# Optimization experiments

Hardware: AMD Instinct MI355X
Metric: run time of the kernel (lower is better)

Reference implementation:

```python
import jax, jax.numpy as jnp
import numpy as np

DIM = 1024
NUM_HEADS = 16
NUM_KV_HEADS = 2
HEAD_DIM = DIM // NUM_HEADS          # 64
REPEATS = NUM_HEADS // NUM_KV_HEADS  # 8
WINDOW = 256
HALF = WINDOW // 2                   # 128
BATCH, SEQ = 2, 2048


def setup_inputs() -> dict:
    key = jax.random.key(0)
    ks = jax.random.split(key, 9)
    sc = 1.0 / np.sqrt(DIM)
    return {
        "x":  jax.random.normal(ks[0], (BATCH, SEQ, DIM), jnp.float32),
        "Wq": jax.random.normal(ks[1], (DIM, NUM_HEADS * HEAD_DIM), jnp.float32) * sc,
        "bq": jax.random.normal(ks[2], (NUM_HEADS * HEAD_DIM,), jnp.float32) * 0.01,
        "Wk": jax.random.normal(ks[3], (DIM, NUM_KV_HEADS * HEAD_DIM), jnp.float32) * sc,
        "bk": jax.random.normal(ks[4], (NUM_KV_HEADS * HEAD_DIM,), jnp.float32) * 0.01,
        "Wv": jax.random.normal(ks[5], (DIM, NUM_KV_HEADS * HEAD_DIM), jnp.float32) * sc,
        "bv": jax.random.normal(ks[6], (NUM_KV_HEADS * HEAD_DIM,), jnp.float32) * 0.01,
        "Wo": jax.random.normal(ks[7], (DIM, DIM), jnp.float32) * sc,
        "bo": jax.random.normal(ks[8], (DIM,), jnp.float32) * 0.01,
    }


def reference(x, Wq, bq, Wk, bk, Wv, bv, Wo, bo):
    # Training-path GQA sliding-window attention (faithful to the torch module):
    #  - K/V zero-padded by HALF on each side of the sequence; window of size
    #    WINDOW centered on each query position (unfold with step 1).
    #  - NOTE (faithful): the original code builds mask = tril(ones)[-1], which is
    #    an all-ones row, so masked_fill is a no-op -> NO causal mask inside the
    #    window; padded positions contribute score 0 (not -inf) to the softmax.
    #  - NOTE (faithful): the training path does NOT scale scores by 1/sqrt(d).
    b, s, _ = x.shape
    q = (x @ Wq + bq).reshape(b, s, NUM_HEADS, HEAD_DIM).transpose(0, 2, 1, 3)      # [b,H,s,d]
    k = (x @ Wk + bk).reshape(b, s, NUM_KV_HEADS, HEAD_DIM).transpose(0, 2, 1, 3)   # [b,G,s,d]
    v = (x @ Wv + bv).reshape(b, s, NUM_KV_HEADS, HEAD_DIM).transpose(0, 2, 1, 3)

    kp = jnp.pad(k, ((0, 0), (0, 0), (HALF, HALF), (0, 0)))  # [b,G,s+W,d]
    vp = jnp.pad(v, ((0, 0), (0, 0), (HALF, HALF), (0, 0)))

    # window gather indices: window i covers padded positions [i, i+W)
    idx = jnp.arange(s)[:, None] + jnp.arange(WINDOW)[None, :]  # [s,W]
    k_win = kp[:, :, idx]  # [b,G,s,W,d]  (gather at kv-head granularity, not H)
    v_win = vp[:, :, idx]

    # group query heads by kv head: head h -> kv group h // REPEATS
    qg = q.reshape(b, NUM_KV_HEADS, REPEATS, s, HEAD_DIM)        # [b,G,r,s,d]
    scores = jnp.einsum('bgrsd,bgswd->bgrsw', qg, k_win)         # no scaling (faithful)
    probs = jax.nn.softmax(scores, axis=-1)
    out = jnp.einsum('bgrsw,bgswd->bgrsd', probs, v_win)         # [b,G,r,s,d]

    out = out.reshape(b, NUM_HEADS, s, HEAD_DIM).transpose(0, 2, 1, 3).reshape(b, s, DIM)
    return out @ Wo + bo
```

## Files before the change

### kernel.cpp

```cpp
#include <hip/hip_runtime.h>
#include <hip/hip_fp16.h>

typedef _Float16 h16;
typedef __attribute__((ext_vector_type(8))) _Float16 h16x8;
typedef __attribute__((ext_vector_type(4))) float f32x4;

#define DIM   1024
#define SEQ   2048
#define NKV   2
#define HD    64
#define HALFW 128
#define NQKV  1280
#define KSTG  288
#define KCOLS 272
#define VCOLS 304
#define VSTR  312

__global__ void preprocess_kernel(const float* __restrict__ x,
                                  const float* __restrict__ bq,
                                  const float* __restrict__ bk,
                                  const float* __restrict__ bv,
                                  const float* __restrict__ Wq,
                                  const float* __restrict__ Wk,
                                  const float* __restrict__ Wv,
                                  const float* __restrict__ Wo,
                                  h16* __restrict__ xh, float* __restrict__ bqkv,
                                  h16* __restrict__ wqkvt, h16* __restrict__ wot)
{
    __shared__ float tile[32][33];
    const int tid = threadIdx.x;
    const int blk = blockIdx.x;
    if (blk < 2048) {
        int i = blk * 256 + tid;
        size_t base = (size_t)i * 8;
        float4 a = *(const float4*)(x + base);
        float4 b = *(const float4*)(x + base + 4);
        h16x8 o = { (h16)a.x,(h16)a.y,(h16)a.z,(h16)a.w,
                    (h16)b.x,(h16)b.y,(h16)b.z,(h16)b.w };
        *(h16x8*)(xh + base) = o;
        if (i < NQKV) {
            float v = (i < DIM) ? bq[i] : (i < DIM+128 ? bk[i-DIM] : bv[i-DIM-128]);
            bqkv[i] = v;
        }
        return;
    }
    const int tx = tid & 31, ty = tid >> 5;
    if (blk < 2048 + 1280) {
        int bid = blk - 2048;
        int n0 = (bid % 40) * 32, k0 = (bid / 40) * 32;
        const float* src; int ldn, noff;
        if (n0 < DIM)          { src = Wq; ldn = DIM; noff = n0; }
        else if (n0 < DIM+128) { src = Wk; ldn = 128; noff = n0 - DIM; }
        else                   { src = Wv; ldn = 128; noff = n0 - DIM - 128; }
#pragma unroll
        for (int i = 0; i < 4; ++i)
            tile[ty + 8*i][tx] = src[(size_t)(k0 + ty + 8*i)*ldn + noff + tx];
        __syncthreads();
#pragma unroll
        for (int i = 0; i < 4; ++i)
            wqkvt[(size_t)(n0 + ty + 8*i)*DIM + k0 + tx] = (h16)tile[tx][ty + 8*i];
    } else {
        int bid = blk - 3328;
        int n0 = (bid % 32) * 32, k0 = (bid / 32) * 32;
#pragma unroll
        for (int i = 0; i < 4; ++i)
            tile[ty + 8*i][tx] = Wo[(size_t)(k0 + ty + 8*i)*DIM + n0 + tx];
        __syncthreads();
#pragma unroll
        for (int i = 0; i < 4; ++i)
            wot[(size_t)(n0 + ty + 8*i)*DIM + k0 + tx] = (h16)tile[tx][ty + 8*i];
    }
}

template<int MODE>
__global__ __launch_bounds__(256, 2)
void gemm_kernel(const h16* __restrict__ A, const h16* __restrict__ Bt,
                 const float* __restrict__ bias,
                 h16* __restrict__ qo, h16* __restrict__ ko, h16* __restrict__ vto,
                 float* __restrict__ co, int K, int nx)
{
    __shared__ __align__(16) h16 As[2][128*64];
    __shared__ __align__(16) h16 Bs[2][128*64];
    const int nwg = gridDim.x, bid = blockIdx.x;
    const int q8 = nwg >> 3, r8 = nwg & 7, xcd = bid & 7, off = bid >> 3;
    const int wg = (xcd < r8 ? xcd*(q8+1) : r8*(q8+1) + (xcd-r8)*q8) + off;
    const int m0 = (wg / nx) * 128, n0 = (wg % nx) * 128;
    const int tid = threadIdx.x, lane = tid & 63, wid = tid >> 6;
    const int wr = wid >> 1, wc = wid & 1;
    f32x4 acc[4][4] = {};

    auto stage = [&](int buf, int kk) {
#pragma unroll
        for (int i = 0; i < 4; ++i) {
            int slot = i*256 + tid;
            int row = slot >> 3;
            int scol = ((slot & 7) ^ (row & 7)) * 8;
            __builtin_amdgcn_global_load_lds(
                (const __attribute__((address_space(1))) void*)(A + (size_t)(m0 + row)*K + kk + scol),
                (__attribute__((address_space(3))) void*)(&As[buf][slot*8]), 16, 0, 0);
            __builtin_amdgcn_global_load_lds(
                (const __attribute__((address_space(1))) void*)(Bt + (size_t)(n0 + row)*K + kk + scol),
                (__attribute__((address_space(3))) void*)(&Bs[buf][slot*8]), 16, 0, 0);
        }
    };
    auto compute = [&](int buf) {
#pragma unroll
        for (int k2 = 0; k2 < 2; ++k2) {
            h16x8 a[4], b[4];
#pragma unroll
            for (int mi = 0; mi < 4; ++mi) {
                int row = wr*64 + mi*16 + (lane & 15);
                int cc = (k2*4 + (lane >> 4)) ^ (row & 7);
                a[mi] = *(const h16x8*)(&As[buf][row*64 + cc*8]);
            }
#pragma unroll
            for (int ni = 0; ni < 4; ++ni) {
                int row = wc*64 + ni*16 + (lane & 15);
                int cc = (k2*4 + (lane >> 4)) ^ (row & 7);
                b[ni] = *(const h16x8*)(&Bs[buf][row*64 + cc*8]);
            }
#pragma unroll
            for (int mi = 0; mi < 4; ++mi)
#pragma unroll
                for (int ni = 0; ni < 4; ++ni)
                    acc[mi][ni] = __builtin_amdgcn_mfma_f32_16x16x32_f16(a[mi], b[ni], acc[mi][ni], 0, 0, 0);
        }
    };

    stage(0, 0);
    __syncthreads();
    int cur = 0;
    for (int kk = 64; kk < K; kk += 64) {
        stage(cur ^ 1, kk);
        compute(cur);
        __syncthreads();
        cur ^= 1;
    }
    compute(cur);

#pragma unroll
    for (int ni = 0; ni < 4; ++ni) {
        int n = n0 + wc*64 + ni*16 + (lane & 15);
        float bv = bias[n];
#pragma unroll
        for (int mi = 0; mi < 4; ++mi) {
            int mb = m0 + wr*64 + mi*16 + (lane >> 4)*4;
#pragma unroll
            for (int r = 0; r < 4; ++r) {
                int m = mb + r;
                float v = acc[mi][ni][r] + bv;
                if (MODE == 1) {
                    co[(size_t)m*DIM + n] = v;
                } else {
                    h16 hv = (h16)v;
                    if (n < DIM) {
                        qo[(size_t)m*DIM + n] = hv;
                    } else {
                        int nn = n - DIM;
                        int bi2 = m >> 11, s = m & 2047;
                        if (nn < 128) {
                            int g = nn >> 6, d = nn & 63;
                            ko[(((size_t)(bi2*NKV + g))*SEQ + s)*HD + d] = hv;
                        } else {
                            nn -= 128;
                            int g = nn >> 6, d = nn & 63;
                            vto[(((size_t)(bi2*NKV + g))*HD + d)*SEQ + s] = hv;
                        }
                    }
                }
            }
        }
    }
}

__global__ __launch_bounds__(512)
void attn_kernel(const h16* __restrict__ qb, const h16* __restrict__ kb,
                 const h16* __restrict__ vtb, h16* __restrict__ ob)
{
    extern __shared__ char smem[];
    h16* Ks  = (h16*)smem;
    h16* Vts = (h16*)(smem + 36864);
    h16* Ps  = (h16*)(smem + 36864 + 39936);
    const int tid = threadIdx.x, lane = tid & 63, wid = tid >> 6;
    const int qt = blockIdx.x, g = blockIdx.y, bi = blockIdx.z;
    const int s0 = qt * 32;
    const size_t kvbase = ((size_t)(bi*NKV + g)) * SEQ * HD;

    for (int slot = tid; slot < KSTG*8; slot += 512) {
        int row = slot >> 3, cc = slot & 7;
        int kpos = s0 - HALFW + row;
        h16x8 val = {0,0,0,0,0,0,0,0};
        if (kpos >= 0 && kpos < SEQ)
            val = *(const h16x8*)(kb + kvbase + (size_t)kpos*HD + cc*8);
        *(h16x8*)(Ks + row*64 + ((cc ^ (row & 7)) * 8)) = val;
    }
    for (int slot = tid; slot < 64*38; slot += 512) {
        int row = slot / 38, cc = slot - row*38;
        int c0 = cc * 8;
        int kp0 = s0 - HALFW + c0;
        const h16* vrow = vtb + kvbase + (size_t)row*SEQ;
        h16x8 val = {0,0,0,0,0,0,0,0};
        if (kp0 >= 0 && kp0 + 8 <= SEQ) {
            val = *(const h16x8*)(vrow + kp0);
        } else {
#pragma unroll
            for (int j = 0; j < 8; ++j) {
                int kp = kp0 + j;
                val[j] = (kp >= 0 && kp < SEQ) ? vrow[kp] : (h16)0;
            }
        }
        *(h16x8*)(Vts + row*VSTR + c0) = val;
    }
    h16* P = Ps + wid * 16 * VSTR;
    for (int i = lane; i < 256; i += 64)
        P[(i >> 4)*VSTR + KCOLS + (i & 15)] = (h16)0;
    __syncthreads();

    const int h = g*8 + wid;
    const int colbase = lane & 15;
    const int rowbase = (lane >> 4) * 4;

    for (int strip = 0; strip < 2; ++strip) {
        const int ss0 = s0 + strip*16;
        h16x8 aq[2];
#pragma unroll
        for (int c = 0; c < 2; ++c)
            aq[c] = *(const h16x8*)(qb + ((size_t)(bi*SEQ + ss0 + colbase))*DIM
                                    + h*HD + c*32 + (lane >> 4)*8);

        f32x4 sc[17];
        __builtin_amdgcn_s_setprio(1);
#pragma unroll
        for (int t = 0; t < 17; ++t) {
            f32x4 z = {0.f,0.f,0.f,0.f};
#pragma unroll
            for (int c = 0; c < 2; ++c) {
                int key = strip*16 + t*16 + colbase;
                h16x8 kf = *(const h16x8*)(Ks + key*64 + (((c*4 + (lane >> 4)) ^ (key & 7)) * 8));
                z = __builtin_amdgcn_mfma_f32_16x16x32_f16(aq[c], kf, z, 0, 0, 0);
            }
            sc[t] = z;
        }
        __builtin_amdgcn_s_setprio(0);

        float mx[4];
#pragma unroll
        for (int r = 0; r < 4; ++r) {
            int row = rowbase + r;
            float v0  = (colbase >= row) ? sc[0][r]  : -1e30f;
            float v16 = (colbase <  row) ? sc[16][r] : -1e30f;
            sc[0][r] = v0; sc[16][r] = v16;
            mx[r] = fmaxf(v0, v16);
        }
#pragma unroll
        for (int t = 1; t < 16; ++t)
#pragma unroll
            for (int r = 0; r < 4; ++r) mx[r] = fmaxf(mx[r], sc[t][r]);
#pragma unroll
        for (int r = 0; r < 4; ++r) {
            mx[r] = fmaxf(mx[r], __shfl_xor(mx[r], 8));
            mx[r] = fmaxf(mx[r], __shfl_xor(mx[r], 4));
            mx[r] = fmaxf(mx[r], __shfl_xor(mx[r], 2));
            mx[r] = fmaxf(mx[r], __shfl_xor(mx[r], 1));
        }
        float sum[4] = {0.f,0.f,0.f,0.f};
#pragma unroll
        for (int t = 0; t < 17; ++t)
#pragma unroll
            for (int r = 0; r < 4; ++r) {
                float p = __expf(sc[t][r] - mx[r]);
                sc[t][r] = p;
                sum[r] += p;
            }
#pragma unroll
        for (int r = 0; r < 4; ++r) {
            sum[r] += __shfl_xor(sum[r], 8);
            sum[r] += __shfl_xor(sum[r], 4);
            sum[r] += __shfl_xor(sum[r], 2);
            sum[r] += __shfl_xor(sum[r], 1);
        }
        float inv[4];
#pragma unroll
        for (int r = 0; r < 4; ++r) inv[r] = 1.0f / sum[r];

#pragma unroll
        for (int t = 0; t < 17; ++t)
#pragma unroll
            for (int r = 0; r < 4; ++r)
                P[(rowbase + r)*VSTR + t*16 + colbase] = (h16)(sc[t][r] * inv[r]);

        f32x4 ao[4] = {};
        __builtin_amdgcn_s_setprio(1);
#pragma unroll
        for (int c = 0; c < 9; ++c) {
            h16x8 pa = *(const h16x8*)(P + colbase*VSTR + c*32 + (lane >> 4)*8);
            int vcol = strip*16 + c*32 + (lane >> 4)*8;
#pragma unroll
            for (int t2 = 0; t2 < 4; ++t2) {
                h16x8 vb = *(const h16x8*)(Vts + (t2*16 + colbase)*VSTR + vcol);
                ao[t2] = __builtin_amdgcn_mfma_f32_16x16x32_f16(pa, vb, ao[t2], 0, 0, 0);
            }
        }
        __builtin_amdgcn_s_setprio(0);
#pragma unroll
        for (int t2 = 0; t2 < 4; ++t2)
#pragma unroll
            for (int r = 0; r < 4; ++r)
                ob[((size_t)(bi*SEQ + ss0 + rowbase + r))*DIM + h*HD + t2*16 + colbase]
                    = (h16)ao[t2][r];
        if (strip == 0) __syncthreads();
    }
}

extern "C" void kernel_launch(void* const* d_in, const int* in_sizes, int n_in,
                              void* d_out, int out_size, void* d_ws, size_t ws_size,
                              hipStream_t stream)
{
    const float* x  = (const float*)d_in[0];
    const float* Wq = (const float*)d_in[1];
    const float* bq = (const float*)d_in[2];
    const float* Wk = (const float*)d_in[3];
    const float* bk = (const float*)d_in[4];
    const float* Wv = (const float*)d_in[5];
    const float* bv = (const float*)d_in[6];
    const float* Wo = (const float*)d_in[7];
    const float* bo = (const float*)d_in[8];
    float* out = (float*)d_out;
    char* ws = (char*)d_ws;

    h16*   xh    = (h16*)(ws);
    h16*   wqkvt = (h16*)(ws + 8388608);
    h16*   wot   = (h16*)(ws + 11010048);
    float* bqkv  = (float*)(ws + 13107200);
    h16*   q_b   = (h16*)(ws + 13112320);
    h16*   k_b   = (h16*)(ws + 21500928);
    h16*   vt_b  = (h16*)(ws + 22549504);
    h16*   att_b = (h16*)(ws + 23598080);

    preprocess_kernel<<<4352, 256, 0, stream>>>(x, bq, bk, bv, Wq, Wk, Wv, Wo,
                                                xh, bqkv, wqkvt, wot);
    gemm_kernel<0><<<320, 256, 0, stream>>>(xh, wqkvt, bqkv,
                                            q_b, k_b, vt_b, nullptr, DIM, 10);
    hipFuncSetAttribute((const void*)attn_kernel,
                        hipFuncAttributeMaxDynamicSharedMemorySize, 156672);
    attn_kernel<<<dim3(64,2,2), 512, 156672, stream>>>(q_b, k_b, vt_b, att_b);
    gemm_kernel<1><<<256, 256, 0, stream>>>(att_b, wot, bo,
                                            nullptr, nullptr, nullptr, out, DIM, 8);
}
```

Baseline: 77.58 us.

## Transpose QK^T MFMA output for lane-local softmax and rework GEMM pipeline barriers

The attention kernel swaps the MFMA operands so each lane holds four keys for a single query. The row max and sum then reduce within the lane and need only two cross-lane shuffles instead of four per row, and P is written with one 4-wide packed store per tile instead of scalar stores. Separately, the GEMM k-loop is restructured to use explicit vmcnt waits and raw s_barrier/sched_barrier in place of __syncthreads. This lets the next stage's loads stay in flight while the current stage computes, but the hand-counted vmcnt(8) is fragile if the number of loads per stage changes.

```diff
diff --git a/kernel.cpp b/kernel.cpp
--- a/kernel.cpp
+++ b/kernel.cpp
@@ -2,6 +2,7 @@
 #include <hip/hip_fp16.h>
 
 typedef _Float16 h16;
+typedef __attribute__((ext_vector_type(4))) _Float16 h16x4;
 typedef __attribute__((ext_vector_type(8))) _Float16 h16x8;
 typedef __attribute__((ext_vector_type(4))) float f32x4;
 
@@ -13,7 +14,6 @@
 #define NQKV  1280
 #define KSTG  288
 #define KCOLS 272
-#define VCOLS 304
 #define VSTR  312
 
 __global__ void preprocess_kernel(const float* __restrict__ x,
@@ -127,16 +127,25 @@
         }
     };
 
+    const int ns = K >> 6;
     stage(0, 0);
-    __syncthreads();
     int cur = 0;
-    for (int kk = 64; kk < K; kk += 64) {
-        stage(cur ^ 1, kk);
+    for (int i = 0; i < ns; ++i) {
+        if (i < ns-1) {
+            stage(cur ^ 1, (i+1) << 6);
+            asm volatile("s_waitcnt vmcnt(8)" ::: "memory");
+        } else {
+            asm volatile("s_waitcnt vmcnt(0)" ::: "memory");
+        }
+        __builtin_amdgcn_s_barrier();
+        __builtin_amdgcn_sched_barrier(0);
         compute(cur);
-        __syncthreads();
+        if (i < ns-1) {
+            __builtin_amdgcn_s_barrier();
+            __builtin_amdgcn_sched_barrier(0);
+        }
         cur ^= 1;
     }
-    compute(cur);
 
 #pragma unroll
     for (int ni = 0; ni < 4; ++ni) {
@@ -219,6 +228,7 @@
     const int h = g*8 + wid;
     const int colbase = lane & 15;
     const int rowbase = (lane >> 4) * 4;
+    const int kg = rowbase;
 
     for (int strip = 0; strip < 2; ++strip) {
         const int ss0 = s0 + strip*16;
@@ -237,57 +247,45 @@
             for (int c = 0; c < 2; ++c) {
                 int key = strip*16 + t*16 + colbase;
                 h16x8 kf = *(const h16x8*)(Ks + key*64 + (((c*4 + (lane >> 4)) ^ (key & 7)) * 8));
-                z = __builtin_amdgcn_mfma_f32_16x16x32_f16(aq[c], kf, z, 0, 0, 0);
+                z = __builtin_amdgcn_mfma_f32_16x16x32_f16(kf, aq[c], z, 0, 0, 0);
             }
             sc[t] = z;
         }
         __builtin_amdgcn_s_setprio(0);
 
-        float mx[4];
+        float mx = -1e30f;
 #pragma unroll
         for (int r = 0; r < 4; ++r) {
-            int row = rowbase + r;
-            float v0  = (colbase >= row) ? sc[0][r]  : -1e30f;
-            float v16 = (colbase <  row) ? sc[16][r] : -1e30f;
+            float v0  = (kg + r >= colbase) ? sc[0][r]  : -1e30f;
+            float v16 = (kg + r <  colbase) ? sc[16][r] : -1e30f;
             sc[0][r] = v0; sc[16][r] = v16;
-            mx[r] = fmaxf(v0, v16);
+            mx = fmaxf(mx, fmaxf(v0, v16));
         }
 #pragma unroll
         for (int t = 1; t < 16; ++t)
 #pragma unroll
-            for (int r = 0; r < 4; ++r) mx[r] = fmaxf(mx[r], sc[t][r]);
-#pragma unroll
-        for (int r = 0; r < 4; ++r) {
-            mx[r] = fmaxf(mx[r], __shfl_xor(mx[r], 8));
-            mx[r] = fmaxf(mx[r], __shfl_xor(mx[r], 4));
-            mx[r] = fmaxf(mx[r], __shfl_xor(mx[r], 2));
-            mx[r] = fmaxf(mx[r], __shfl_xor(mx[r], 1));
-        }
-        float sum[4] = {0.f,0.f,0.f,0.f};
+            for (int r = 0; r < 4; ++r) mx = fmaxf(mx, sc[t][r]);
+        mx = fmaxf(mx, __shfl_xor(mx, 16));
+        mx = fmaxf(mx, __shfl_xor(mx, 32));
+        float sum = 0.f;
 #pragma unroll
         for (int t = 0; t < 17; ++t)
 #pragma unroll
             for (int r = 0; r < 4; ++r) {
-                float p = __expf(sc[t][r] - mx[r]);
+                float p = __expf(sc[t][r] - mx);
                 sc[t][r] = p;
-                sum[r] += p;
-            }
-#pragma unroll
-        for (int r = 0; r < 4; ++r) {
-            sum[r] += __shfl_xor(sum[r], 8);
-            sum[r] += __shfl_xor(sum[r], 4);
-            sum[r] += __shfl_xor(sum[r], 2);
-            sum[r] += __shfl_xor(sum[r], 1);
-        }
-        float inv[4];
-#pragma unroll
-        for (int r = 0; r < 4; ++r) inv[r] = 1.0f / sum[r];
-
-#pragma unroll
-        for (int t = 0; t < 17; ++t)
-#pragma unroll
-            for (int r = 0; r < 4; ++r)
-                P[(rowbase + r)*VSTR + t*16 + colbase] = (h16)(sc[t][r] * inv[r]);
+                sum += p;
+            }
+        sum += __shfl_xor(sum, 16);
+        sum += __shfl_xor(sum, 32);
+        float inv = 1.0f / sum;
+
+#pragma unroll
+        for (int t = 0; t < 17; ++t) {
+            h16x4 pk = { (h16)(sc[t][0]*inv), (h16)(sc[t][1]*inv),
+                         (h16)(sc[t][2]*inv), (h16)(sc[t][3]*inv) };
+            *(h16x4*)(P + colbase*VSTR + t*16 + kg) = pk;
+        }
 
         f32x4 ao[4] = {};
         __builtin_amdgcn_s_setprio(1);
```

After: 76.20 us. No clear change (-1.8%).
